# Kernel optimization log

Hardware: AMD Instinct MI355X
Metric: run time of the kernel (lower is better)

Reference implementation:

```python
import jax, jax.numpy as jnp
import numpy as np
import math

N = 8192
D = 256


def _lorentz_linear(x, W, b, log_scale):
    # x: [N, D] -> linear -> project onto Lorentz manifold
    y = x @ W.T + b                                    # [N, D]
    time = jax.nn.sigmoid(y[:, :1]) * jnp.exp(log_scale) + 1.1   # [N, 1]
    spatial = y[:, 1:]                                 # [N, D-1]
    sq = jnp.clip(jnp.sum(spatial * spatial, axis=-1, keepdims=True), 1e-8)
    scale = (time * time - 1.0) / sq                   # [N, 1]
    return jnp.concatenate([time, spatial * jnp.sqrt(scale)], axis=-1)


def setup_inputs() -> dict:
    key = jax.random.key(0)
    ks = jax.random.split(key, 7)
    stdv = 1.0 / math.sqrt(D)
    x = jax.random.normal(ks[0], (N, D), dtype=jnp.float32)
    Wq = jax.random.uniform(ks[1], (D, D), jnp.float32, -stdv, stdv).at[:, 0].set(0.0)
    bq = jnp.zeros((D,), jnp.float32)
    sq_log = jnp.asarray(math.log(10.0), jnp.float32)   # LorentzLinear scale param
    Wk = jax.random.uniform(ks[2], (D, D), jnp.float32, -stdv, stdv).at[:, 0].set(0.0)
    bk = jnp.zeros((D,), jnp.float32)
    sk_log = jnp.asarray(math.log(10.0), jnp.float32)
    att_bias = jnp.asarray(20.0, jnp.float32)
    att_scale = jnp.asarray(math.sqrt(D), jnp.float32)
    return {"x": x, "Wq": Wq, "bq": bq, "sq_log": sq_log,
            "Wk": Wk, "bk": bk, "sk_log": sk_log,
            "att_bias": att_bias, "att_scale": att_scale}


def reference(x, Wq, bq, sq_log, Wk, bk, sk_log, att_bias, att_scale):
    query = _lorentz_linear(x, Wq, bq, sq_log)   # [N, D]
    key = _lorentz_linear(x, Wk, bk, sk_log)     # [N, D]
    # Minkowski inner product: -q0*k0 + sum_i qi*ki = q@k^T - 2*q0 k0^T
    cin = query @ key.T - 2.0 * jnp.outer(query[:, 0], key[:, 0])   # [N, N]
    att_adj = jax.nn.sigmoid((2.0 + 2.0 * cin) / att_scale + att_bias)
    support = att_adj @ x                        # [N, D]
    # denorm = sqrt(clamp(|-inner(u,u)|)) with inner = -u0^2 + sum spatial^2
    neg_inner = support[:, :1] ** 2 - jnp.sum(support[:, 1:] ** 2, axis=-1, keepdims=True)
    denorm = jnp.sqrt(jnp.clip(jnp.abs(neg_inner), 1e-8))
    output = support / denorm
    return output, att_adj
```

## Files before the change

### kernel.cpp

```cpp
#include <hip/hip_runtime.h>
#include <hip/hip_bf16.h>

#define N_ROWS 8192
#define D_DIM  256

typedef __attribute__((ext_vector_type(8))) short bf16x8;
typedef __attribute__((ext_vector_type(4))) float f32x4;

__device__ __forceinline__ unsigned short f2bf(float x) {
    unsigned u = __float_as_uint(x);
    u = (u + 0x7FFFu + ((u >> 16) & 1u)) >> 16;
    return (unsigned short)u;
}
__device__ __forceinline__ float bf2f(unsigned short u) {
    return __uint_as_float(((unsigned)u) << 16);
}
__device__ __forceinline__ f32x4 mfma16(bf16x8 a, bf16x8 b, f32x4 c) {
    return __builtin_amdgcn_mfma_f32_16x16x32_bf16(a, b, c, 0, 0, 0);
}

__global__ __launch_bounds__(256) void prep_kernel(
    const float* __restrict__ x, const float* __restrict__ Wq, const float* __restrict__ Wk,
    unsigned short* __restrict__ xhi, unsigned short* __restrict__ xlo,
    unsigned short* __restrict__ Xt,
    unsigned short* __restrict__ Wqh, unsigned short* __restrict__ Wql,
    unsigned short* __restrict__ Wkh, unsigned short* __restrict__ Wkl)
{
    __shared__ unsigned short tile[64 * 256];
    int b = blockIdx.x, t = threadIdx.x;
    if (b < 128) {
        int rowbase = b * 64;
        int c = t >> 2, f0 = (t & 3) * 64;
        const float* xp = x + (size_t)(rowbase + c) * D_DIM + f0;
        size_t gbase = (size_t)(rowbase + c) * D_DIM + f0;
#pragma unroll
        for (int i = 0; i < 8; ++i) {
            float4 a4 = *(const float4*)(xp + 8 * i);
            float4 b4 = *(const float4*)(xp + 8 * i + 4);
            float v[8] = {a4.x, a4.y, a4.z, a4.w, b4.x, b4.y, b4.z, b4.w};
            bf16x8 hv, lv;
#pragma unroll
            for (int j = 0; j < 8; ++j) {
                unsigned short h = f2bf(v[j]);
                hv[j] = (short)h;
                lv[j] = (short)f2bf(v[j] - bf2f(h));
            }
            *(bf16x8*)(xhi + gbase + 8 * i) = hv;
            *(bf16x8*)(xlo + gbase + 8 * i) = lv;
            *(bf16x8*)(&tile[c * 256 + (((f0 + 8 * i) ^ ((c & 7) << 3)))]) = hv;
        }
        __syncthreads();
        int f = t;
        unsigned short vals[64];
#pragma unroll
        for (int c2 = 0; c2 < 64; ++c2)
            vals[c2] = tile[c2 * 256 + (f ^ ((c2 & 7) << 3))];
#pragma unroll
        for (int i = 0; i < 8; ++i) {
            bf16x8 pv;
#pragma unroll
            for (int j = 0; j < 8; ++j) pv[j] = (short)vals[8 * i + j];
            *(bf16x8*)(Xt + (size_t)f * N_ROWS + rowbase + 8 * i) = pv;
        }
    } else {
        int wb = b - 128;
        const float* src = (wb < 4) ? Wq : Wk;
        unsigned short* dh = (wb < 4) ? Wqh : Wkh;
        unsigned short* dl = (wb < 4) ? Wql : Wkl;
        int base = (wb & 3) * 16384;
#pragma unroll 4
        for (int i = 0; i < 64; ++i) {
            int idx = base + i * 256 + t;
            float v = src[idx];
            unsigned short h = f2bf(v);
            dh[idx] = h;
            dl[idx] = f2bf(v - bf2f(h));
        }
    }
}

__global__ __launch_bounds__(64) void qk_kernel(
    const unsigned short* __restrict__ xhi, const unsigned short* __restrict__ xlo,
    const unsigned short* __restrict__ Wh, const unsigned short* __restrict__ Wl,
    const float* __restrict__ bias, const float* __restrict__ logscale,
    unsigned short* __restrict__ Qb, float* __restrict__ q0)
{
    int lane = threadIdx.x;
    int rowb = blockIdx.x * 16;
    int m = lane & 15, g = lane >> 4;

    bf16x8 ah[8], al[8];
    size_t abase = (size_t)(rowb + m) * D_DIM + g * 8;
#pragma unroll
    for (int k = 0; k < 8; ++k) {
        ah[k] = *(const bf16x8*)(xhi + abase + k * 32);
        al[k] = *(const bf16x8*)(xlo + abase + k * 32);
    }
    f32x4 acc[16];
#pragma unroll
    for (int fn = 0; fn < 16; ++fn) {
        f32x4 a = (f32x4){0.f, 0.f, 0.f, 0.f};
        size_t wbase = (size_t)(fn * 16 + m) * D_DIM + g * 8;
#pragma unroll
        for (int k = 0; k < 8; ++k) {
            bf16x8 bh = *(const bf16x8*)(Wh + wbase + k * 32);
            bf16x8 bl = *(const bf16x8*)(Wl + wbase + k * 32);
            a = mfma16(ah[k], bh, a);
            a = mfma16(ah[k], bl, a);
            a = mfma16(al[k], bh, a);
        }
        acc[fn] = a;
    }
    float es = expf(logscale[0]);
#pragma unroll
    for (int fn = 0; fn < 16; ++fn) {
        float bv = bias[fn * 16 + m];
#pragma unroll
        for (int r = 0; r < 4; ++r) acc[fn][r] += bv;
    }
#pragma unroll
    for (int r = 0; r < 4; ++r) {
        float p = 0.f;
#pragma unroll
        for (int fn = 0; fn < 16; ++fn) { float v = acc[fn][r]; p += v * v; }
        if (m == 0) p -= acc[0][r] * acc[0][r];
        p += __shfl_xor(p, 1);
        p += __shfl_xor(p, 2);
        p += __shfl_xor(p, 4);
        p += __shfl_xor(p, 8);
        float y0 = __shfl(acc[0][r], g * 16);
        float tt = es / (1.f + expf(-y0)) + 1.1f;
        float ssq = fmaxf(p, 1e-8f);
        float s = sqrtf((tt * tt - 1.f) / ssq);
        int row = rowb + g * 4 + r;
#pragma unroll
        for (int fn = 0; fn < 16; ++fn) {
            float v = acc[fn][r] * s;
            Qb[(size_t)row * D_DIM + fn * 16 + m] =
                (fn == 0 && m == 0) ? (unsigned short)0 : f2bf(v);
        }
        if (m == 0) q0[row] = tt;
    }
}

__global__ __launch_bounds__(512, 2) void att_kernel(
    const unsigned short* __restrict__ Qb, const unsigned short* __restrict__ Kb,
    const float* __restrict__ q0, const float* __restrict__ k0,
    const unsigned short* __restrict__ Xt,
    const float* __restrict__ p_scale, const float* __restrict__ p_bias,
    float* __restrict__ att_out, float* __restrict__ partial, int chunkW)
{
    __shared__ unsigned short Ks[64 * 256];
    __shared__ unsigned short Xs[256 * 64];
    int tid = threadIdx.x;
    int lane = tid & 63, wid = tid >> 6;
    int wm = wid >> 1, wn = wid & 1;
    int m16 = lane & 15, g = lane >> 4;
    int rowbase = blockIdx.x * 128;
    int colbase = blockIdx.y * chunkW;
    float as = p_scale[0], ab = p_bias[0];

    bf16x8 qa[2][8];
#pragma unroll
    for (int mi = 0; mi < 2; ++mi) {
        size_t base = (size_t)(rowbase + wm * 32 + mi * 16 + m16) * D_DIM + g * 8;
#pragma unroll
        for (int k = 0; k < 8; ++k)
            qa[mi][k] = *(const bf16x8*)(Qb + base + k * 32);
    }
    float q0v[2][4];
#pragma unroll
    for (int mi = 0; mi < 2; ++mi)
#pragma unroll
        for (int r = 0; r < 4; ++r)
            q0v[mi][r] = q0[rowbase + wm * 32 + mi * 16 + g * 4 + r];

    f32x4 oacc[2][8];
#pragma unroll
    for (int mi = 0; mi < 2; ++mi)
#pragma unroll
        for (int n = 0; n < 8; ++n)
            oacc[mi][n] = (f32x4){0.f, 0.f, 0.f, 0.f};

    int nstrips = chunkW / 64;
    int sc = tid >> 3, sko = (tid & 7) * 32;
    int sf = tid >> 1, sco = (tid & 1) * 32;

    for (int s = 0; s < nstrips; ++s) {
        int cb = colbase + s * 64;
        if (s) __syncthreads();
        {
            const unsigned short* srcK = Kb + (size_t)(cb + sc) * D_DIM + sko;
            unsigned short* dK = Ks + sc * 256;
            int swK = (sc & 7) << 3;
#pragma unroll
            for (int i = 0; i < 4; ++i)
                *(bf16x8*)(dK + ((sko + 8 * i) ^ swK)) = *(const bf16x8*)(srcK + 8 * i);
            const unsigned short* srcX = Xt + (size_t)sf * N_ROWS + cb + sco;
            unsigned short* dX = Xs + sf * 64;
            int swX = (sf & 7) << 3;
#pragma unroll
            for (int i = 0; i < 4; ++i)
                *(bf16x8*)(dX + ((sco + 8 * i) ^ swX)) = *(const bf16x8*)(srcX + 8 * i);
        }
        __syncthreads();

        f32x4 sacc[2][2];
#pragma unroll
        for (int mi = 0; mi < 2; ++mi)
#pragma unroll
            for (int fn = 0; fn < 2; ++fn)
                sacc[mi][fn] = (f32x4){0.f, 0.f, 0.f, 0.f};
#pragma unroll
        for (int k = 0; k < 8; ++k) {
            bf16x8 bk[2];
#pragma unroll
            for (int fn = 0; fn < 2; ++fn) {
                int row = wn * 32 + fn * 16 + m16;
                bk[fn] = *(const bf16x8*)(Ks + row * 256 + (((k * 32 + g * 8)) ^ ((row & 7) << 3)));
            }
#pragma unroll
            for (int mi = 0; mi < 2; ++mi)
#pragma unroll
                for (int fn = 0; fn < 2; ++fn)
                    sacc[mi][fn] = mfma16(qa[mi][k], bk[fn], sacc[mi][fn]);
        }
        __syncthreads();

        float k0v[2];
#pragma unroll
        for (int fn = 0; fn < 2; ++fn)
            k0v[fn] = k0[cb + wn * 32 + fn * 16 + m16];
        unsigned short* As = Ks;
#pragma unroll
        for (int mi = 0; mi < 2; ++mi)
#pragma unroll
            for (int fn = 0; fn < 2; ++fn)
#pragma unroll
                for (int r = 0; r < 4; ++r) {
                    float cin = sacc[mi][fn][r] - q0v[mi][r] * k0v[fn];
                    float z = (2.f + 2.f * cin) / as + ab;
                    float attv = 1.f / (1.f + expf(-z));
                    int row = wm * 32 + mi * 16 + g * 4 + r;
                    int col = wn * 32 + fn * 16 + m16;
                    att_out[(size_t)(rowbase + row) * N_ROWS + cb + col] = attv;
                    As[row * 64 + (col ^ ((row & 7) << 3))] = f2bf(attv);
                }
        __syncthreads();

#pragma unroll
        for (int kf = 0; kf < 2; ++kf) {
            bf16x8 pa[2];
#pragma unroll
            for (int mi = 0; mi < 2; ++mi) {
                int row = wm * 32 + mi * 16 + m16;
                pa[mi] = *(const bf16x8*)(As + row * 64 + (((kf * 32 + g * 8)) ^ ((row & 7) << 3)));
            }
#pragma unroll
            for (int n = 0; n < 8; ++n) {
                int f = wn * 128 + n * 16 + m16;
                bf16x8 xb = *(const bf16x8*)(Xs + f * 64 + (((kf * 32 + g * 8)) ^ ((f & 7) << 3)));
#pragma unroll
                for (int mi = 0; mi < 2; ++mi)
                    oacc[mi][n] = mfma16(pa[mi], xb, oacc[mi][n]);
            }
        }
    }

    float* pbase = partial + (size_t)blockIdx.y * N_ROWS * D_DIM;
#pragma unroll
    for (int mi = 0; mi < 2; ++mi)
#pragma unroll
        for (int n = 0; n < 8; ++n)
#pragma unroll
            for (int r = 0; r < 4; ++r) {
                int row = rowbase + wm * 32 + mi * 16 + g * 4 + r;
                int f = wn * 128 + n * 16 + m16;
                pbase[(size_t)row * D_DIM + f] = oacc[mi][n][r];
            }
}

__global__ __launch_bounds__(64) void norm_kernel(
    const float* __restrict__ partial, float* __restrict__ outp, int nchunk)
{
    int row = blockIdx.x, lane = threadIdx.x;
    float a0 = 0.f, a1 = 0.f, a2 = 0.f, a3 = 0.f;
    for (int p = 0; p < nchunk; ++p) {
        const float4 v = *(const float4*)(partial + ((size_t)p * N_ROWS + row) * D_DIM + lane * 4);
        a0 += v.x; a1 += v.y; a2 += v.z; a3 += v.w;
    }
    float sq = a0 * a0 + a1 * a1 + a2 * a2 + a3 * a3;
#pragma unroll
    for (int off = 1; off < 64; off <<= 1) sq += __shfl_xor(sq, off);
    float s0 = __shfl(a0, 0);
    float neg = 2.f * s0 * s0 - sq;
    float dn = sqrtf(fmaxf(fabsf(neg), 1e-8f));
    float inv = 1.f / dn;
    float4 o;
    o.x = a0 * inv; o.y = a1 * inv; o.z = a2 * inv; o.w = a3 * inv;
    *(float4*)(outp + (size_t)row * D_DIM + lane * 4) = o;
}

extern "C" void kernel_launch(void* const* d_in, const int* in_sizes, int n_in,
                              void* d_out, int out_size, void* d_ws, size_t ws_size,
                              hipStream_t stream)
{
    const float* x         = (const float*)d_in[0];
    const float* Wq        = (const float*)d_in[1];
    const float* bq        = (const float*)d_in[2];
    const float* sq_log    = (const float*)d_in[3];
    const float* Wk        = (const float*)d_in[4];
    const float* bk        = (const float*)d_in[5];
    const float* sk_log    = (const float*)d_in[6];
    const float* att_bias  = (const float*)d_in[7];
    const float* att_scale = (const float*)d_in[8];
    float* outp    = (float*)d_out;
    float* att_out = outp + (size_t)N_ROWS * D_DIM;

    char* w = (char*)d_ws;
    size_t used = 0;
    auto alloc = [&](size_t bytes) -> char* {
        char* p = w + used;
        used += (bytes + 255) & ~(size_t)255;
        return p;
    };
    unsigned short* xhi = (unsigned short*)alloc((size_t)N_ROWS * D_DIM * 2);
    unsigned short* xlo = (unsigned short*)alloc((size_t)N_ROWS * D_DIM * 2);
    unsigned short* XtB = (unsigned short*)alloc((size_t)N_ROWS * D_DIM * 2);
    unsigned short* Wqh = (unsigned short*)alloc((size_t)65536 * 2);
    unsigned short* Wql = (unsigned short*)alloc((size_t)65536 * 2);
    unsigned short* Wkh = (unsigned short*)alloc((size_t)65536 * 2);
    unsigned short* Wkl = (unsigned short*)alloc((size_t)65536 * 2);
    unsigned short* QbB = (unsigned short*)alloc((size_t)N_ROWS * D_DIM * 2);
    unsigned short* KbB = (unsigned short*)alloc((size_t)N_ROWS * D_DIM * 2);
    float* q0v = (float*)alloc((size_t)N_ROWS * 4);
    float* k0v = (float*)alloc((size_t)N_ROWS * 4);

    int nchunk = 4;
    while (nchunk > 1 &&
           used + (size_t)nchunk * N_ROWS * D_DIM * 4 > ws_size)
        nchunk >>= 1;
    float* partial = (float*)alloc((size_t)nchunk * N_ROWS * D_DIM * 4);

    hipLaunchKernelGGL(prep_kernel, dim3(136), dim3(256), 0, stream,
                       x, Wq, Wk, xhi, xlo, XtB, Wqh, Wql, Wkh, Wkl);
    hipLaunchKernelGGL(qk_kernel, dim3(N_ROWS / 16), dim3(64), 0, stream,
                       xhi, xlo, Wqh, Wql, bq, sq_log, QbB, q0v);
    hipLaunchKernelGGL(qk_kernel, dim3(N_ROWS / 16), dim3(64), 0, stream,
                       xhi, xlo, Wkh, Wkl, bk, sk_log, KbB, k0v);
    int chunkW = N_ROWS / nchunk;
    hipLaunchKernelGGL(att_kernel, dim3(N_ROWS / 128, nchunk), dim3(512), 0, stream,
                       QbB, KbB, q0v, k0v, XtB, att_scale, att_bias,
                       att_out, partial, chunkW);
    hipLaunchKernelGGL(norm_kernel, dim3(N_ROWS), dim3(64), 0, stream,
                       partial, outp, nchunk);
}
```

Measured before the change: 507.8 us.

## Retile attention kernel to 64-row blocks, transpose score MFMA, split qk across waves

The attention kernel now processes 64 query rows per block with a 2x4 wave grid and launch bounds allowing 4 blocks per CU, so more blocks are resident and the grid is larger. The score MFMA is transposed (K as A operand) so each lane holds 4 consecutive columns, which lets it write att_out with float4 stores and pack bf16 values into 8-byte LDS stores. The sigmoid is simplified with precomputed constants, fast exp and a hardware reciprocal. The qk kernel splits its 16 output fragments across 4 waves and reduces the norms through shared memory, adding parallelism in exchange for a barrier. The trade-off is that K and X strips are reloaded into LDS by twice as many blocks, doubling that traffic.

Result: slower. 624.8 us (+23.1%).

```diff
diff --git a/kernel.cpp b/kernel.cpp
--- a/kernel.cpp
+++ b/kernel.cpp
@@ -79,13 +79,16 @@
     }
 }
 
-__global__ __launch_bounds__(64) void qk_kernel(
+__global__ __launch_bounds__(256) void qk_kernel(
     const unsigned short* __restrict__ xhi, const unsigned short* __restrict__ xlo,
     const unsigned short* __restrict__ Wh, const unsigned short* __restrict__ Wl,
     const float* __restrict__ bias, const float* __restrict__ logscale,
     unsigned short* __restrict__ Qb, float* __restrict__ q0)
 {
-    int lane = threadIdx.x;
+    __shared__ float red[4][16];
+    __shared__ float y0s[16];
+    int tid = threadIdx.x;
+    int lane = tid & 63, w = tid >> 6;
     int rowb = blockIdx.x * 16;
     int m = lane & 15, g = lane >> 4;
 
@@ -96,9 +99,10 @@
         ah[k] = *(const bf16x8*)(xhi + abase + k * 32);
         al[k] = *(const bf16x8*)(xlo + abase + k * 32);
     }
-    f32x4 acc[16];
-#pragma unroll
-    for (int fn = 0; fn < 16; ++fn) {
+    f32x4 acc[4];
+#pragma unroll
+    for (int fnl = 0; fnl < 4; ++fnl) {
+        int fn = w * 4 + fnl;
         f32x4 a = (f32x4){0.f, 0.f, 0.f, 0.f};
         size_t wbase = (size_t)(fn * 16 + m) * D_DIM + g * 8;
 #pragma unroll
@@ -109,41 +113,53 @@
             a = mfma16(ah[k], bl, a);
             a = mfma16(al[k], bh, a);
         }
-        acc[fn] = a;
-    }
-    float es = expf(logscale[0]);
-#pragma unroll
-    for (int fn = 0; fn < 16; ++fn) {
         float bv = bias[fn * 16 + m];
 #pragma unroll
-        for (int r = 0; r < 4; ++r) acc[fn][r] += bv;
-    }
+        for (int r = 0; r < 4; ++r) a[r] += bv;
+        acc[fnl] = a;
+    }
+    float p[4];
 #pragma unroll
     for (int r = 0; r < 4; ++r) {
-        float p = 0.f;
-#pragma unroll
-        for (int fn = 0; fn < 16; ++fn) { float v = acc[fn][r]; p += v * v; }
-        if (m == 0) p -= acc[0][r] * acc[0][r];
-        p += __shfl_xor(p, 1);
-        p += __shfl_xor(p, 2);
-        p += __shfl_xor(p, 4);
-        p += __shfl_xor(p, 8);
-        float y0 = __shfl(acc[0][r], g * 16);
-        float tt = es / (1.f + expf(-y0)) + 1.1f;
-        float ssq = fmaxf(p, 1e-8f);
-        float s = sqrtf((tt * tt - 1.f) / ssq);
-        int row = rowb + g * 4 + r;
-#pragma unroll
-        for (int fn = 0; fn < 16; ++fn) {
-            float v = acc[fn][r] * s;
+        float s = 0.f;
+#pragma unroll
+        for (int fnl = 0; fnl < 4; ++fnl) { float v = acc[fnl][r]; s += v * v; }
+        if (w == 0 && m == 0) s -= acc[0][r] * acc[0][r];
+        s += __shfl_xor(s, 1);
+        s += __shfl_xor(s, 2);
+        s += __shfl_xor(s, 4);
+        s += __shfl_xor(s, 8);
+        p[r] = s;
+    }
+    if (m == 0) {
+#pragma unroll
+        for (int r = 0; r < 4; ++r) red[w][g * 4 + r] = p[r];
+        if (w == 0)
+#pragma unroll
+            for (int r = 0; r < 4; ++r) y0s[g * 4 + r] = acc[0][r];
+    }
+    __syncthreads();
+    float es = __expf(logscale[0]);
+#pragma unroll
+    for (int r = 0; r < 4; ++r) {
+        int rr = g * 4 + r;
+        float ssq = red[0][rr] + red[1][rr] + red[2][rr] + red[3][rr];
+        float y0 = y0s[rr];
+        float tt = es * __builtin_amdgcn_rcpf(1.f + __expf(-y0)) + 1.1f;
+        float sc = sqrtf((tt * tt - 1.f) * __builtin_amdgcn_rcpf(fmaxf(ssq, 1e-8f)));
+        int row = rowb + rr;
+#pragma unroll
+        for (int fnl = 0; fnl < 4; ++fnl) {
+            int fn = w * 4 + fnl;
+            float v = acc[fnl][r] * sc;
             Qb[(size_t)row * D_DIM + fn * 16 + m] =
                 (fn == 0 && m == 0) ? (unsigned short)0 : f2bf(v);
         }
-        if (m == 0) q0[row] = tt;
-    }
-}
-
-__global__ __launch_bounds__(512, 2) void att_kernel(
+        if (w == 0 && m == 0) q0[row] = tt;
+    }
+}
+
+__global__ __launch_bounds__(512, 4) void att_kernel(
     const unsigned short* __restrict__ Qb, const unsigned short* __restrict__ Kb,
     const float* __restrict__ q0, const float* __restrict__ k0,
     const unsigned short* __restrict__ Xt,
@@ -154,11 +170,12 @@
     __shared__ unsigned short Xs[256 * 64];
     int tid = threadIdx.x;
     int lane = tid & 63, wid = tid >> 6;
-    int wm = wid >> 1, wn = wid & 1;
+    int wm = wid >> 2, wn = wid & 3;
     int m16 = lane & 15, g = lane >> 4;
-    int rowbase = blockIdx.x * 128;
+    int rowbase = blockIdx.x * 64;
     int colbase = blockIdx.y * chunkW;
-    float as = p_scale[0], ab = p_bias[0];
+    float c1 = 2.0f / p_scale[0];
+    float c0 = c1 + p_bias[0];
 
     bf16x8 qa[2][8];
 #pragma unroll
@@ -168,23 +185,22 @@
         for (int k = 0; k < 8; ++k)
             qa[mi][k] = *(const bf16x8*)(Qb + base + k * 32);
     }
-    float q0v[2][4];
+    float q0v[2];
 #pragma unroll
     for (int mi = 0; mi < 2; ++mi)
-#pragma unroll
-        for (int r = 0; r < 4; ++r)
-            q0v[mi][r] = q0[rowbase + wm * 32 + mi * 16 + g * 4 + r];
-
-    f32x4 oacc[2][8];
+        q0v[mi] = q0[rowbase + wm * 32 + mi * 16 + m16];
+
+    f32x4 oacc[2][4];
 #pragma unroll
     for (int mi = 0; mi < 2; ++mi)
 #pragma unroll
-        for (int n = 0; n < 8; ++n)
+        for (int n = 0; n < 4; ++n)
             oacc[mi][n] = (f32x4){0.f, 0.f, 0.f, 0.f};
 
     int nstrips = chunkW / 64;
     int sc = tid >> 3, sko = (tid & 7) * 32;
     int sf = tid >> 1, sco = (tid & 1) * 32;
+    unsigned short* As = Ks;
 
     for (int s = 0; s < nstrips; ++s) {
         int cb = colbase + s * 64;
@@ -205,47 +221,37 @@
         }
         __syncthreads();
 
-        f32x4 sacc[2][2];
-#pragma unroll
-        for (int mi = 0; mi < 2; ++mi)
-#pragma unroll
-            for (int fn = 0; fn < 2; ++fn)
-                sacc[mi][fn] = (f32x4){0.f, 0.f, 0.f, 0.f};
+        f32x4 sacc[2];
+        sacc[0] = (f32x4){0.f, 0.f, 0.f, 0.f};
+        sacc[1] = (f32x4){0.f, 0.f, 0.f, 0.f};
+        int krow = wn * 16 + m16;
+        int swk = (krow & 7) << 3;
 #pragma unroll
         for (int k = 0; k < 8; ++k) {
-            bf16x8 bk[2];
-#pragma unroll
-            for (int fn = 0; fn < 2; ++fn) {
-                int row = wn * 32 + fn * 16 + m16;
-                bk[fn] = *(const bf16x8*)(Ks + row * 256 + (((k * 32 + g * 8)) ^ ((row & 7) << 3)));
-            }
-#pragma unroll
-            for (int mi = 0; mi < 2; ++mi)
-#pragma unroll
-                for (int fn = 0; fn < 2; ++fn)
-                    sacc[mi][fn] = mfma16(qa[mi][k], bk[fn], sacc[mi][fn]);
+            bf16x8 kb = *(const bf16x8*)(Ks + krow * 256 + ((k * 32 + g * 8) ^ swk));
+            sacc[0] = mfma16(kb, qa[0][k], sacc[0]);
+            sacc[1] = mfma16(kb, qa[1][k], sacc[1]);
         }
         __syncthreads();
 
-        float k0v[2];
-#pragma unroll
-        for (int fn = 0; fn < 2; ++fn)
-            k0v[fn] = k0[cb + wn * 32 + fn * 16 + m16];
-        unsigned short* As = Ks;
-#pragma unroll
-        for (int mi = 0; mi < 2; ++mi)
-#pragma unroll
-            for (int fn = 0; fn < 2; ++fn)
-#pragma unroll
-                for (int r = 0; r < 4; ++r) {
-                    float cin = sacc[mi][fn][r] - q0v[mi][r] * k0v[fn];
-                    float z = (2.f + 2.f * cin) / as + ab;
-                    float attv = 1.f / (1.f + expf(-z));
-                    int row = wm * 32 + mi * 16 + g * 4 + r;
-                    int col = wn * 32 + fn * 16 + m16;
-                    att_out[(size_t)(rowbase + row) * N_ROWS + cb + col] = attv;
-                    As[row * 64 + (col ^ ((row & 7) << 3))] = f2bf(attv);
-                }
+        float4 k0v = *(const float4*)(k0 + cb + wn * 16 + g * 4);
+#pragma unroll
+        for (int mi = 0; mi < 2; ++mi) {
+            int qrow = wm * 32 + mi * 16 + m16;
+            float av[4];
+#pragma unroll
+            for (int r = 0; r < 4; ++r) {
+                float cin = sacc[mi][r] - q0v[mi] * (&k0v.x)[r];
+                float z = c0 + c1 * cin;
+                av[r] = __builtin_amdgcn_rcpf(1.f + __expf(-z));
+            }
+            *(float4*)(att_out + (size_t)(rowbase + qrow) * N_ROWS + cb + wn * 16 + g * 4) =
+                (float4){av[0], av[1], av[2], av[3]};
+            uint2 pk;
+            pk.x = (unsigned)f2bf(av[0]) | ((unsigned)f2bf(av[1]) << 16);
+            pk.y = (unsigned)f2bf(av[2]) | ((unsigned)f2bf(av[3]) << 16);
+            *(uint2*)(As + qrow * 64 + ((wn * 16 + g * 4) ^ ((qrow & 7) << 3))) = pk;
+        }
         __syncthreads();
 
 #pragma unroll
@@ -257,8 +263,8 @@
                 pa[mi] = *(const bf16x8*)(As + row * 64 + (((kf * 32 + g * 8)) ^ ((row & 7) << 3)));
             }
 #pragma unroll
-            for (int n = 0; n < 8; ++n) {
-                int f = wn * 128 + n * 16 + m16;
+            for (int n = 0; n < 4; ++n) {
+                int f = wn * 64 + n * 16 + m16;
                 bf16x8 xb = *(const bf16x8*)(Xs + f * 64 + (((kf * 32 + g * 8)) ^ ((f & 7) << 3)));
 #pragma unroll
                 for (int mi = 0; mi < 2; ++mi)
@@ -271,11 +277,11 @@
 #pragma unroll
     for (int mi = 0; mi < 2; ++mi)
 #pragma unroll
-        for (int n = 0; n < 8; ++n)
+        for (int n = 0; n < 4; ++n)
 #pragma unroll
             for (int r = 0; r < 4; ++r) {
                 int row = rowbase + wm * 32 + mi * 16 + g * 4 + r;
-                int f = wn * 128 + n * 16 + m16;
+                int f = wn * 64 + n * 16 + m16;
                 pbase[(size_t)row * D_DIM + f] = oacc[mi][n][r];
             }
 }
@@ -344,12 +350,12 @@
 
     hipLaunchKernelGGL(prep_kernel, dim3(136), dim3(256), 0, stream,
                        x, Wq, Wk, xhi, xlo, XtB, Wqh, Wql, Wkh, Wkl);
-    hipLaunchKernelGGL(qk_kernel, dim3(N_ROWS / 16), dim3(64), 0, stream,
+    hipLaunchKernelGGL(qk_kernel, dim3(N_ROWS / 16), dim3(256), 0, stream,
                        xhi, xlo, Wqh, Wql, bq, sq_log, QbB, q0v);
-    hipLaunchKernelGGL(qk_kernel, dim3(N_ROWS / 16), dim3(64), 0, stream,
+    hipLaunchKernelGGL(qk_kernel, dim3(N_ROWS / 16), dim3(256), 0, stream,
                        xhi, xlo, Wkh, Wkl, bk, sk_log, KbB, k0v);
     int chunkW = N_ROWS / nchunk;
-    hipLaunchKernelGGL(att_kernel, dim3(N_ROWS / 128, nchunk), dim3(512), 0, stream,
+    hipLaunchKernelGGL(att_kernel, dim3(N_ROWS / 64, nchunk), dim3(512), 0, stream,
                        QbB, KbB, q0v, k0v, XtB, att_scale, att_bias,
                        att_out, partial, chunkW);
     hipLaunchKernelGGL(norm_kernel, dim3(N_ROWS), dim3(64), 0, stream,
```
